# Kernel optimization log

Hardware: AMD Instinct MI355X
Metric: run time of the kernel (lower is better)

Reference implementation:

```python
import jax, jax.numpy as jnp
import numpy as np

# Dimensions
B_, L_, D_ = 2, 1024, 1024
EXPAND, N_STATE, K_CONV = 2, 16, 4
D_INNER = D_ * EXPAND          # 2048
DT_RANK = (D_ + 15) // 16      # 64 (mamba default: ceil(d_model/16))


def setup_inputs() -> dict:
    key = jax.random.key(0)
    ks = jax.random.split(key, 10)
    sc = 0.02
    x = jax.random.normal(ks[0], (B_, L_, D_), jnp.float32)
    ln_w = jnp.ones((D_,), jnp.float32)
    ln_b = jnp.zeros((D_,), jnp.float32)
    W_in = jax.random.normal(ks[1], (2 * D_INNER, D_), jnp.float32) * sc
    W_conv = jax.random.normal(ks[2], (D_INNER, K_CONV), jnp.float32) * 0.2
    b_conv = jnp.zeros((D_INNER,), jnp.float32)
    W_xproj = jax.random.normal(ks[3], (DT_RANK + 2 * N_STATE, D_INNER), jnp.float32) * sc
    W_dt = jax.random.normal(ks[4], (D_INNER, DT_RANK), jnp.float32) * (DT_RANK ** -0.5)
    # dt bias: inverse softplus of dt ~ U[1e-3, 1e-1] (mamba init)
    dt = jnp.exp(jax.random.uniform(ks[5], (D_INNER,), jnp.float32)
                 * (np.log(0.1) - np.log(0.001)) + np.log(0.001))
    b_dt = dt + jnp.log(-jnp.expm1(-dt))
    # A_log init: log(1..N) per channel (S4D-real init)
    A_log = jnp.log(jnp.broadcast_to(jnp.arange(1, N_STATE + 1, dtype=jnp.float32),
                                     (D_INNER, N_STATE)))
    D_skip = jnp.ones((D_INNER,), jnp.float32)
    W_out = jax.random.normal(ks[6], (D_, D_INNER), jnp.float32) * sc
    return {"x": x, "ln_w": ln_w, "ln_b": ln_b, "W_in": W_in, "W_conv": W_conv,
            "b_conv": b_conv, "W_xproj": W_xproj, "W_dt": W_dt, "b_dt": b_dt,
            "A_log": A_log, "D_skip": D_skip, "W_out": W_out}


def _layernorm(x, w, b, eps=1e-5):
    mu = jnp.mean(x, axis=-1, keepdims=True)
    var = jnp.mean(jnp.square(x - mu), axis=-1, keepdims=True)
    return (x - mu) * jax.lax.rsqrt(var + eps) * w + b


def reference(x, ln_w, ln_b, W_in, W_conv, b_conv, W_xproj, W_dt, b_dt,
              A_log, D_skip, W_out):
    B, L, D = x.shape
    residual = x
    xn = _layernorm(x, ln_w, ln_b)

    # in_proj -> (x_ssm, z), each (B, L, d_inner)
    xz = jnp.einsum('bld,ed->ble', xn, W_in)
    xs, z = jnp.split(xz, 2, axis=-1)

    # causal depthwise conv1d along L + SiLU
    xp = jnp.pad(xs, ((0, 0), (K_CONV - 1, 0), (0, 0)))
    xc = b_conv + sum(xp[:, k:k + L, :] * W_conv[:, k] for k in range(K_CONV))
    xc = jax.nn.silu(xc)

    # input-dependent dt, B, C
    dbl = jnp.einsum('ble,re->blr', xc, W_xproj)
    dt_low = dbl[..., :DT_RANK]
    B_ssm = dbl[..., DT_RANK:DT_RANK + N_STATE]        # (B, L, N)
    C_ssm = dbl[..., DT_RANK + N_STATE:]               # (B, L, N)
    delta = jax.nn.softplus(jnp.einsum('blr,er->ble', dt_low, W_dt) + b_dt)  # (B, L, d_inner)

    A = -jnp.exp(A_log)                                # (d_inner, N)
    dA = jnp.exp(delta[..., None] * A)                 # (B, L, d_inner, N)
    dBx = delta[..., None] * B_ssm[:, :, None, :] * xc[..., None]  # (B, L, d_inner, N)

    def step(h, inp):
        dA_t, dBx_t, C_t = inp
        h = dA_t * h + dBx_t                           # (B, d_inner, N)
        y_t = jnp.einsum('bdn,bn->bd', h, C_t)
        return h, y_t

    h0 = jnp.zeros((B, D_INNER, N_STATE), x.dtype)
    _, ys = jax.lax.scan(step, h0,
                         (dA.transpose(1, 0, 2, 3), dBx.transpose(1, 0, 2, 3),
                          C_ssm.transpose(1, 0, 2)))
    y = ys.transpose(1, 0, 2) + D_skip * xc            # (B, L, d_inner)
    y = y * jax.nn.silu(z)
    out = jnp.einsum('ble,de->bld', y, W_out)
    # dropout is identity in eval mode
    return out + residual
```

## Files before the change

kernel.cpp:

```cpp
#include <hip/hip_runtime.h>
#include <math.h>

#define B_ 2
#define L_ 1024
#define D_ 1024
#define D_INNER 2048
#define DT_RANK 64
#define N_STATE 16
#define NC 64
#define LC 16

typedef __attribute__((ext_vector_type(8))) short bf16x8;
typedef __attribute__((ext_vector_type(4))) float f32x4;

__device__ __forceinline__ unsigned short f2bf(float f) {
  unsigned int u = __float_as_uint(f);
  u += 0x7fffu + ((u >> 16) & 1u);
  return (unsigned short)(u >> 16);
}
__device__ __forceinline__ float bf2f(unsigned short s) {
  return __uint_as_float((unsigned int)s << 16);
}
__device__ __forceinline__ float softplus_f(float v) {
  return (v > 20.0f) ? v : log1pf(__expf(v));
}

#define N4_WIN  1048576
#define N4_WOUT  524288
#define N4_WDT    32768
#define N4_WXP    65536
#define N4_ZERO   49152
#define N4_CPY   524288
#define PREP_F4 (N4_WIN + N4_WOUT + N4_WDT + N4_WXP + N4_ZERO + N4_CPY)
#define PREP_BLOCKS (2048 + (PREP_F4 + 255) / 256)

__global__ __launch_bounds__(256) void prep_kernel(const float* __restrict__ x,
                                                   const float* __restrict__ w,
                                                   const float* __restrict__ b,
                                                   unsigned short* __restrict__ xn_b,
                                                   const float* __restrict__ W_in,
                                                   const float* __restrict__ W_out,
                                                   const float* __restrict__ W_dt,
                                                   const float* __restrict__ W_xp,
                                                   unsigned short* __restrict__ Win_b,
                                                   unsigned short* __restrict__ Wout_b,
                                                   unsigned short* __restrict__ Wdt_b,
                                                   unsigned short* __restrict__ Wxp_b,
                                                   float* __restrict__ dblb,
                                                   float* __restrict__ outb) {
  if (blockIdx.x < 2048) {
    int row = blockIdx.x;
    int tid = threadIdx.x;
    const float* xr = x + (size_t)row * D_;
    float4 v = ((const float4*)xr)[tid];
    float s  = v.x + v.y + v.z + v.w;
    float s2 = v.x*v.x + v.y*v.y + v.z*v.z + v.w*v.w;
    #pragma unroll
    for (int off = 32; off > 0; off >>= 1) {
      s  += __shfl_down(s, off);
      s2 += __shfl_down(s2, off);
    }
    __shared__ float ss[4], ss2[4];
    int wid = tid >> 6, lane = tid & 63;
    if (lane == 0) { ss[wid] = s; ss2[wid] = s2; }
    __syncthreads();
    if (tid == 0) {
      float a  = ss[0] + ss[1] + ss[2] + ss[3];
      float a2 = ss2[0] + ss2[1] + ss2[2] + ss2[3];
      ss[0]  = a  * (1.0f / D_);
      ss2[0] = a2 * (1.0f / D_);
    }
    __syncthreads();
    float mu = ss[0];
    float var = ss2[0] - mu * mu;
    float rstd = rsqrtf(var + 1e-5f);
    float4 wv = ((const float4*)w)[tid];
    float4 bv = ((const float4*)b)[tid];
    ushort4 o;
    o.x = f2bf((v.x - mu) * rstd * wv.x + bv.x);
    o.y = f2bf((v.y - mu) * rstd * wv.y + bv.y);
    o.z = f2bf((v.z - mu) * rstd * wv.z + bv.z);
    o.w = f2bf((v.w - mu) * rstd * wv.w + bv.w);
    ((ushort4*)(xn_b + (size_t)row * D_))[tid] = o;
    return;
  }
  int i = (blockIdx.x - 2048) * 256 + threadIdx.x;
  if (i < N4_WIN) {
    float4 v = ((const float4*)W_in)[i];
    ushort4 o; o.x = f2bf(v.x); o.y = f2bf(v.y); o.z = f2bf(v.z); o.w = f2bf(v.w);
    ((ushort4*)Win_b)[i] = o;
    return;
  }
  i -= N4_WIN;
  if (i < N4_WOUT) {
    float4 v = ((const float4*)W_out)[i];
    ushort4 o; o.x = f2bf(v.x); o.y = f2bf(v.y); o.z = f2bf(v.z); o.w = f2bf(v.w);
    ((ushort4*)Wout_b)[i] = o;
    return;
  }
  i -= N4_WOUT;
  if (i < N4_WDT) {
    float4 v = ((const float4*)W_dt)[i];
    ushort4 o; o.x = f2bf(v.x); o.y = f2bf(v.y); o.z = f2bf(v.z); o.w = f2bf(v.w);
    ((ushort4*)Wdt_b)[i] = o;
    return;
  }
  i -= N4_WDT;
  if (i < N4_WXP) {
    int row = (i * 4) >> 11;
    ushort4 o = make_ushort4(0, 0, 0, 0);
    if (row < 96) {
      float4 v = ((const float4*)W_xp)[i];
      o.x = f2bf(v.x); o.y = f2bf(v.y); o.z = f2bf(v.z); o.w = f2bf(v.w);
    }
    ((ushort4*)Wxp_b)[i] = o;
    return;
  }
  i -= N4_WXP;
  if (i < N4_ZERO) {
    ((float4*)dblb)[i] = make_float4(0.f, 0.f, 0.f, 0.f);
    return;
  }
  i -= N4_ZERO;
  if (i < N4_CPY) {
    ((float4*)outb)[i] = ((const float4*)x)[i];
  }
}

template<int EPI, int BMT>
__global__ __launch_bounds__(256) void gemm_mfma(const unsigned short* __restrict__ A, int lda,
                                                 const unsigned short* __restrict__ B, int ldb,
                                                 float* __restrict__ Cf,
                                                 unsigned short* __restrict__ Cb,
                                                 int ldc, int Nguard, int K,
                                                 const float* __restrict__ ep0,
                                                 const float* __restrict__ Af32 = nullptr) {
  __shared__ unsigned short As[BMT * 64];
  __shared__ unsigned short Bs[128 * 64];
  const int tid = threadIdx.x;
  const int lane = tid & 63;
  const int w = tid >> 6;
  const int wr = w >> 1, wc = w & 1;
  int flat = blockIdx.y * gridDim.x + blockIdx.x;
  int nwg = gridDim.x * gridDim.y;
  int q8 = nwg >> 3;
  int swz = (flat & 7) * q8 + (flat >> 3);
  const int bm = (swz / gridDim.x) * BMT;
  const int bn = (swz % gridDim.x) * 128;
  const int l16 = lane & 15;
  constexpr int MW = BMT / 32;

  int kbeg = 0, kend = K;
  if (EPI == 4 || EPI == 7) {
    int ks = K / gridDim.z;
    kbeg = blockIdx.z * ks;
    kend = kbeg + ks;
  }

  f32x4 acc[MW][4];
  #pragma unroll
  for (int m = 0; m < MW; ++m)
    #pragma unroll
    for (int n = 0; n < 4; ++n) acc[m][n] = (f32x4){0.f, 0.f, 0.f, 0.f};

  for (int k0 = kbeg; k0 < kend; k0 += 64) {
    if constexpr (EPI == 5) {
      #pragma unroll
      for (int i = 0; i < BMT / 32; ++i) {
        int p = (i * 256 + tid) * 16;
        int r = p >> 7;
        int s = (p >> 4) & 7;
        int cb = ((s ^ (r & 7)) << 3);
        const float* ga = Af32 + (size_t)(bm + r) * lda + cb;
        float4 v0 = *(const float4*)ga;
        float4 v1 = *(const float4*)(ga + 4);
        ushort4 u0 = make_ushort4(f2bf(v0.x), f2bf(v0.y), f2bf(v0.z), f2bf(v0.w));
        ushort4 u1 = make_ushort4(f2bf(v1.x), f2bf(v1.y), f2bf(v1.z), f2bf(v1.w));
        *(ushort4*)(As + (p >> 1)) = u0;
        *(ushort4*)(As + (p >> 1) + 4) = u1;
      }
    } else {
      #pragma unroll
      for (int i = 0; i < BMT / 32; ++i) {
        int p = (i * 256 + tid) * 16;
        int r = p >> 7;
        int s = (p >> 4) & 7;
        int cb = ((s ^ (r & 7)) << 3);
        const unsigned short* ga = A + (size_t)(bm + r) * lda + k0 + cb;
        __builtin_amdgcn_global_load_lds(
            (const __attribute__((address_space(1))) void*)ga,
            (__attribute__((address_space(3))) void*)(As + (p >> 1)), 16, 0, 0);
      }
    }
    #pragma unroll
    for (int i = 0; i < 4; ++i) {
      int p = (i * 256 + tid) * 16;
      int r = p >> 7;
      int s = (p >> 4) & 7;
      int cb = ((s ^ (r & 7)) << 3);
      const unsigned short* gb = B + (size_t)(bn + r) * ldb + k0 + cb;
      __builtin_amdgcn_global_load_lds(
          (const __attribute__((address_space(1))) void*)gb,
          (__attribute__((address_space(3))) void*)(Bs + (p >> 1)), 16, 0, 0);
    }
    __syncthreads();
    #pragma unroll
    for (int ks = 0; ks < 2; ++ks) {
      const int slot = ks * 4 + (lane >> 4);
      bf16x8 af[MW], bfr[4];
      #pragma unroll
      for (int m = 0; m < MW; ++m) {
        int ar = wr * (BMT / 2) + m * 16 + l16;
        af[m] = *(const bf16x8*)(As + ar * 64 + ((slot ^ (ar & 7)) << 3));
      }
      #pragma unroll
      for (int n = 0; n < 4; ++n) {
        int br = wc * 64 + n * 16 + l16;
        bfr[n] = *(const bf16x8*)(Bs + br * 64 + ((slot ^ (br & 7)) << 3));
      }
      #pragma unroll
      for (int m = 0; m < MW; ++m)
        #pragma unroll
        for (int n = 0; n < 4; ++n)
          acc[m][n] = __builtin_amdgcn_mfma_f32_16x16x32_bf16(af[m], bfr[n], acc[m][n], 0, 0, 0);
    }
    __syncthreads();
  }

  const int crow0 = bm + wr * (BMT / 2) + (lane >> 4) * 4;
  const int ccol0 = bn + wc * 64 + l16;
  #pragma unroll
  for (int m = 0; m < MW; ++m) {
    #pragma unroll
    for (int n = 0; n < 4; ++n) {
      int c = ccol0 + n * 16;
      if (c >= Nguard) continue;
      #pragma unroll
      for (int r = 0; r < 4; ++r) {
        int rr = crow0 + m * 16 + r;
        float v = acc[m][n][r];
        if (EPI == 1) {
          Cb[(size_t)rr * ldc + c] = f2bf(v);
        } else if (EPI == 4 || EPI == 7) {
          atomicAdd(&Cf[(size_t)rr * ldc + c], v);
        } else if (EPI == 5) {
          Cb[(size_t)rr * ldc + c] = f2bf(softplus_f(v + ep0[c]));
        } else {
          Cf[(size_t)rr * ldc + c] = v;
        }
      }
    }
  }
}

__global__ __launch_bounds__(256) void conv_silu_kernel(const unsigned short* __restrict__ xz,
                                                        const float* __restrict__ Wc,
                                                        const float* __restrict__ bc,
                                                        unsigned short* __restrict__ xcb) {
  int idx = blockIdx.x * 256 + threadIdx.x;
  int e = idx & (D_INNER - 1);
  int t = (idx >> 11) & (L_ - 1);
  int bt = idx >> 11;
  float acc = bc[e];
  float w0 = Wc[e * 4 + 0], w1 = Wc[e * 4 + 1], w2 = Wc[e * 4 + 2], w3 = Wc[e * 4 + 3];
  const unsigned short* base = xz + (size_t)bt * 4096 + e;
  if (t >= 3) acc = fmaf(bf2f(base[-3 * 4096]), w0, acc);
  if (t >= 2) acc = fmaf(bf2f(base[-2 * 4096]), w1, acc);
  if (t >= 1) acc = fmaf(bf2f(base[-1 * 4096]), w2, acc);
  acc = fmaf(bf2f(base[0]), w3, acc);
  float s = acc / (1.0f + __expf(-acc));
  xcb[idx] = f2bf(s);
}

__global__ __launch_bounds__(256) void scan1_kernel(const unsigned short* __restrict__ delta,
                                                    const unsigned short* __restrict__ xc,
                                                    const float* __restrict__ dbl,
                                                    const float* __restrict__ A_log,
                                                    float* __restrict__ P,
                                                    float* __restrict__ Q) {
  int e = blockIdx.x * 256 + threadIdx.x;
  int b = blockIdx.y, c = blockIdx.z;
  const int t0 = (int)(b * L_ + c * LC);

  __shared__ float sB[LC][N_STATE];
  {
    int step = threadIdx.x >> 4, n = threadIdx.x & 15;
    sB[step][n] = dbl[(size_t)(t0 + step) * 96 + 64 + n];
  }
  __syncthreads();

  float An[N_STATE];
  #pragma unroll
  for (int q = 0; q < 4; ++q) {
    float4 v = *(const float4*)&A_log[(size_t)e * N_STATE + q * 4];
    An[q*4+0] = -__expf(v.x); An[q*4+1] = -__expf(v.y);
    An[q*4+2] = -__expf(v.z); An[q*4+3] = -__expf(v.w);
  }
  float h[N_STATE], p[N_STATE];
  #pragma unroll
  for (int n = 0; n < N_STATE; ++n) { h[n] = 0.f; p[n] = 1.f; }

  const size_t row0 = (size_t)t0 * D_INNER + e;
  float dlt = bf2f(delta[row0]);
  float xcv = bf2f(xc[row0]);

  for (int tt = 0; tt < LC; ++tt) {
    float ndlt = 0.f, nxcv = 0.f;
    if (tt + 1 < LC) {
      ndlt = bf2f(delta[row0 + (size_t)(tt + 1) * D_INNER]);
      nxcv = bf2f(xc[row0 + (size_t)(tt + 1) * D_INNER]);
    }
    float dbx = dlt * xcv;
    #pragma unroll
    for (int n = 0; n < N_STATE; ++n) {
      float da = __expf(dlt * An[n]);
      h[n] = fmaf(da, h[n], dbx * sB[tt][n]);
      p[n] *= da;
    }
    dlt = ndlt; xcv = nxcv;
  }
  size_t o = ((size_t)(c * B_ + b) * N_STATE) * D_INNER + e;
  #pragma unroll
  for (int n = 0; n < N_STATE; ++n) {
    P[o + (size_t)n * D_INNER] = p[n];
    Q[o + (size_t)n * D_INNER] = h[n];
  }
}

__global__ __launch_bounds__(256) void scan2_kernel(const float* __restrict__ P,
                                                    float* __restrict__ Q) {
  int idx = blockIdx.x * 256 + threadIdx.x;
  float H = 0.f;
  #pragma unroll
  for (int c = 0; c < NC; ++c) {
    size_t o = (size_t)c * (B_ * N_STATE * D_INNER) + idx;
    float p = P[o], q = Q[o];
    Q[o] = H;
    H = fmaf(p, H, q);
  }
}

__global__ __launch_bounds__(256) void scan3_kernel(const unsigned short* __restrict__ delta,
                                                    const unsigned short* __restrict__ xc,
                                                    const float* __restrict__ dbl,
                                                    const float* __restrict__ A_log,
                                                    const float* __restrict__ Hinit,
                                                    const unsigned short* __restrict__ xz,
                                                    const float* __restrict__ Dsk,
                                                    unsigned short* __restrict__ y) {
  int e = blockIdx.x * 256 + threadIdx.x;
  int b = blockIdx.y, c = blockIdx.z;
  const int t0 = (int)(b * L_ + c * LC);

  __shared__ float sB[LC][N_STATE];
  __shared__ float sC[LC][N_STATE];
  {
    int step = threadIdx.x >> 4, n = threadIdx.x & 15;
    const float* row = dbl + (size_t)(t0 + step) * 96;
    sB[step][n] = row[64 + n];
    sC[step][n] = row[80 + n];
  }
  __syncthreads();

  float An[N_STATE];
  #pragma unroll
  for (int q = 0; q < 4; ++q) {
    float4 v = *(const float4*)&A_log[(size_t)e * N_STATE + q * 4];
    An[q*4+0] = -__expf(v.x); An[q*4+1] = -__expf(v.y);
    An[q*4+2] = -__expf(v.z); An[q*4+3] = -__expf(v.w);
  }
  float h[N_STATE];
  {
    size_t o = ((size_t)(c * B_ + b) * N_STATE) * D_INNER + e;
    #pragma unroll
    for (int n = 0; n < N_STATE; ++n) h[n] = Hinit[o + (size_t)n * D_INNER];
  }
  float dskip = Dsk[e];
  const size_t row0 = (size_t)t0 * D_INNER + e;
  const size_t zrow0 = (size_t)t0 * 4096 + D_INNER + e;

  float dlt = bf2f(delta[row0]);
  float xcv = bf2f(xc[row0]);
  float zv  = bf2f(xz[zrow0]);

  for (int tt = 0; tt < LC; ++tt) {
    float ndlt = 0.f, nxcv = 0.f, nzv = 0.f;
    if (tt + 1 < LC) {
      ndlt = bf2f(delta[row0 + (size_t)(tt + 1) * D_INNER]);
      nxcv = bf2f(xc[row0 + (size_t)(tt + 1) * D_INNER]);
      nzv  = bf2f(xz[zrow0 + (size_t)(tt + 1) * 4096]);
    }
    float dbx = dlt * xcv;
    float yv = 0.f;
    #pragma unroll
    for (int n = 0; n < N_STATE; ++n) {
      float da = __expf(dlt * An[n]);
      h[n] = fmaf(da, h[n], dbx * sB[tt][n]);
      yv = fmaf(h[n], sC[tt][n], yv);
    }
    float gate = zv / (1.0f + __expf(-zv));
    y[row0 + (size_t)tt * D_INNER] = f2bf((yv + dskip * xcv) * gate);
    dlt = ndlt; xcv = nxcv; zv = nzv;
  }
}

extern "C" void kernel_launch(void* const* d_in, const int* in_sizes, int n_in,
                              void* d_out, int out_size, void* d_ws, size_t ws_size,
                              hipStream_t stream) {
  const float* x       = (const float*)d_in[0];
  const float* ln_w    = (const float*)d_in[1];
  const float* ln_b    = (const float*)d_in[2];
  const float* W_in    = (const float*)d_in[3];
  const float* W_conv  = (const float*)d_in[4];
  const float* b_conv  = (const float*)d_in[5];
  const float* W_xproj = (const float*)d_in[6];
  const float* W_dt    = (const float*)d_in[7];
  const float* b_dt    = (const float*)d_in[8];
  const float* A_log   = (const float*)d_in[9];
  const float* D_skip  = (const float*)d_in[10];
  const float* W_out   = (const float*)d_in[11];
  float* out = (float*)d_out;

  const size_t BL = (size_t)B_ * L_;
  float* dblb = (float*)d_ws;
  float* P    = dblb + 196608;
  float* Q    = P    + 4194304;
  unsigned short* xn_b    = (unsigned short*)(Q + 4194304);
  unsigned short* Win_b   = xn_b    + 2097152;
  unsigned short* xz_b    = Win_b   + 4194304;
  unsigned short* xc_b    = xz_b    + 8388608;
  unsigned short* Wxp_b   = xc_b    + 4194304;
  unsigned short* y_b     = Wxp_b   + 262144;
  unsigned short* Wout_b  = y_b     + 4194304;
  unsigned short* Wdt_b   = Wout_b  + 2097152;
  unsigned short* delta_b = Wdt_b   + 131072;

  prep_kernel<<<PREP_BLOCKS, 256, 0, stream>>>(
      x, ln_w, ln_b, xn_b, W_in, W_out, W_dt, W_xproj,
      Win_b, Wout_b, Wdt_b, Wxp_b, dblb, out);
  gemm_mfma<1, 128><<<dim3(32, 16), 256, 0, stream>>>(
      xn_b, D_, Win_b, D_, nullptr, xz_b, 4096, 4096, D_, nullptr);
  conv_silu_kernel<<<(BL * D_INNER) / 256, 256, 0, stream>>>(xz_b, W_conv, b_conv, xc_b);
  gemm_mfma<4, 128><<<dim3(1, 16, 16), 256, 0, stream>>>(
      xc_b, D_INNER, Wxp_b, D_INNER, dblb, nullptr, 96, 96, D_INNER, nullptr);
  gemm_mfma<5, 128><<<dim3(16, 16), 256, 0, stream>>>(
      nullptr, 96, Wdt_b, DT_RANK, nullptr, delta_b, D_INNER, D_INNER, DT_RANK, b_dt, dblb);
  scan1_kernel<<<dim3(D_INNER / 256, B_, NC), 256, 0, stream>>>(delta_b, xc_b, dblb, A_log, P, Q);
  scan2_kernel<<<(B_ * N_STATE * D_INNER) / 256, 256, 0, stream>>>(P, Q);
  scan3_kernel<<<dim3(D_INNER / 256, B_, NC), 256, 0, stream>>>(delta_b, xc_b, dblb, A_log, Q,
                                                                xz_b, D_skip, y_b);
  gemm_mfma<7, 64><<<dim3(8, 32, 2), 256, 0, stream>>>(
      y_b, D_INNER, Wout_b, D_INNER, out, nullptr, D_, D_, D_INNER, nullptr);
}
```

Measured before the change: 258.1 us.

## Fuse causal conv1d+SiLU into x_proj GEMM A-tile load, retile in_proj GEMM

Removes the standalone conv_silu kernel and computes the depthwise causal conv plus SiLU while staging the A tile of the split-K x_proj GEMM, writing xc to global as a side output for the scan kernels. This saves one launch and a full read/write pass of xc. In exchange, A-tile loads become synchronous vector loads with ALU work instead of async global-to-LDS copies, and reads four rows of xz per element. The in_proj GEMM also switches to 64-row tiles with twice the blocks.

```diff
diff --git a/kernel.cpp b/kernel.cpp
--- a/kernel.cpp
+++ b/kernel.cpp
@@ -151,7 +151,7 @@
   constexpr int MW = BMT / 32;
 
   int kbeg = 0, kend = K;
-  if (EPI == 4 || EPI == 7) {
+  if (EPI == 6 || EPI == 7) {
     int ks = K / gridDim.z;
     kbeg = blockIdx.z * ks;
     kend = kbeg + ks;
@@ -179,6 +179,42 @@
         *(ushort4*)(As + (p >> 1)) = u0;
         *(ushort4*)(As + (p >> 1) + 4) = u1;
       }
+    } else if constexpr (EPI == 6) {
+      #pragma unroll
+      for (int i = 0; i < BMT / 32; ++i) {
+        int p = (i * 256 + tid) * 16;
+        int r = p >> 7;
+        int s = (p >> 4) & 7;
+        int cb = ((s ^ (r & 7)) << 3);
+        int tg = bm + r;
+        int tt = tg & (L_ - 1);
+        int e  = k0 + cb;
+        const unsigned short* bp = A + (size_t)tg * lda + e;
+        bf16x8 x0 = *(const bf16x8*)bp;
+        bf16x8 xm1 = (bf16x8)(short)0, xm2 = (bf16x8)(short)0, xm3 = (bf16x8)(short)0;
+        if (tt >= 1) xm1 = *(const bf16x8*)(bp - lda);
+        if (tt >= 2) xm2 = *(const bf16x8*)(bp - 2 * lda);
+        if (tt >= 3) xm3 = *(const bf16x8*)(bp - 3 * lda);
+        unsigned short res[8];
+        #pragma unroll
+        for (int j = 0; j < 8; ++j) {
+          float4 wv = ((const float4*)Af32)[e + j];
+          float a = ep0[e + j];
+          a = fmaf(bf2f((unsigned short)xm3[j]), wv.x, a);
+          a = fmaf(bf2f((unsigned short)xm2[j]), wv.y, a);
+          a = fmaf(bf2f((unsigned short)xm1[j]), wv.z, a);
+          a = fmaf(bf2f((unsigned short)x0[j]),  wv.w, a);
+          float sv = a / (1.0f + __expf(-a));
+          res[j] = f2bf(sv);
+        }
+        ushort4 u0 = make_ushort4(res[0], res[1], res[2], res[3]);
+        ushort4 u1 = make_ushort4(res[4], res[5], res[6], res[7]);
+        *(ushort4*)(As + (p >> 1)) = u0;
+        *(ushort4*)(As + (p >> 1) + 4) = u1;
+        unsigned short* xo = Cb + (size_t)tg * D_INNER + e;
+        *(ushort4*)xo = u0;
+        *(ushort4*)(xo + 4) = u1;
+      }
     } else {
       #pragma unroll
       for (int i = 0; i < BMT / 32; ++i) {
@@ -241,7 +277,7 @@
         float v = acc[m][n][r];
         if (EPI == 1) {
           Cb[(size_t)rr * ldc + c] = f2bf(v);
-        } else if (EPI == 4 || EPI == 7) {
+        } else if (EPI == 6 || EPI == 7) {
           atomicAdd(&Cf[(size_t)rr * ldc + c], v);
         } else if (EPI == 5) {
           Cb[(size_t)rr * ldc + c] = f2bf(softplus_f(v + ep0[c]));
@@ -251,25 +287,6 @@
       }
     }
   }
-}
-
-__global__ __launch_bounds__(256) void conv_silu_kernel(const unsigned short* __restrict__ xz,
-                                                        const float* __restrict__ Wc,
-                                                        const float* __restrict__ bc,
-                                                        unsigned short* __restrict__ xcb) {
-  int idx = blockIdx.x * 256 + threadIdx.x;
-  int e = idx & (D_INNER - 1);
-  int t = (idx >> 11) & (L_ - 1);
-  int bt = idx >> 11;
-  float acc = bc[e];
-  float w0 = Wc[e * 4 + 0], w1 = Wc[e * 4 + 1], w2 = Wc[e * 4 + 2], w3 = Wc[e * 4 + 3];
-  const unsigned short* base = xz + (size_t)bt * 4096 + e;
-  if (t >= 3) acc = fmaf(bf2f(base[-3 * 4096]), w0, acc);
-  if (t >= 2) acc = fmaf(bf2f(base[-2 * 4096]), w1, acc);
-  if (t >= 1) acc = fmaf(bf2f(base[-1 * 4096]), w2, acc);
-  acc = fmaf(bf2f(base[0]), w3, acc);
-  float s = acc / (1.0f + __expf(-acc));
-  xcb[idx] = f2bf(s);
 }
 
 __global__ __launch_bounds__(256) void scan1_kernel(const unsigned short* __restrict__ delta,
@@ -438,11 +455,10 @@
   prep_kernel<<<PREP_BLOCKS, 256, 0, stream>>>(
       x, ln_w, ln_b, xn_b, W_in, W_out, W_dt, W_xproj,
       Win_b, Wout_b, Wdt_b, Wxp_b, dblb, out);
-  gemm_mfma<1, 128><<<dim3(32, 16), 256, 0, stream>>>(
+  gemm_mfma<1, 64><<<dim3(32, 32), 256, 0, stream>>>(
       xn_b, D_, Win_b, D_, nullptr, xz_b, 4096, 4096, D_, nullptr);
-  conv_silu_kernel<<<(BL * D_INNER) / 256, 256, 0, stream>>>(xz_b, W_conv, b_conv, xc_b);
-  gemm_mfma<4, 128><<<dim3(1, 16, 16), 256, 0, stream>>>(
-      xc_b, D_INNER, Wxp_b, D_INNER, dblb, nullptr, 96, 96, D_INNER, nullptr);
+  gemm_mfma<6, 128><<<dim3(1, 16, 16), 256, 0, stream>>>(
+      xz_b, 4096, Wxp_b, D_INNER, dblb, xc_b, 96, 96, D_INNER, b_conv, W_conv);
   gemm_mfma<5, 128><<<dim3(16, 16), 256, 0, stream>>>(
       nullptr, 96, Wdt_b, DT_RANK, nullptr, delta_b, D_INNER, D_INNER, DT_RANK, b_dt, dblb);
   scan1_kernel<<<dim3(D_INNER / 256, B_, NC), 256, 0, stream>>>(delta_b, xc_b, dblb, A_log, P, Q);
```

New measurement: 250.5 us. 2.9% less time.
